# Kernel optimization log

Hardware: AMD Instinct MI355X
Metric: run time of the kernel (lower is better)

## Reference

```python
import jax, jax.numpy as jnp
import numpy as np

BETA = 0.95
THR = 1.0  # snntorch Leaky default threshold

# Heaviside spike with ATan surrogate gradient (snntorch default, alpha=2):
# d/dx = 1 / (1 + (pi*x)^2)
@jax.custom_vjp
def spike_fn(x):
    return (x > 0).astype(x.dtype)

def _spike_fwd(x):
    return spike_fn(x), x

def _spike_bwd(x, g):
    return (g / (1.0 + (jnp.pi * x) ** 2),)

spike_fn.defvjp(_spike_fwd, _spike_bwd)


def setup_inputs() -> dict:
    key = jax.random.key(0)
    ks = jax.random.split(key, 5)
    T, B, D_in, D_h, D_out = 25, 4096, 784, 1000, 10
    x = jax.random.normal(ks[0], (T, B, D_in), dtype=jnp.float32)
    # Kaiming-uniform-ish init like nn.Linear
    w1 = jax.random.uniform(ks[1], (D_h, D_in), jnp.float32, -1, 1) / np.sqrt(D_in)
    b1 = jax.random.uniform(ks[2], (D_h,), jnp.float32, -1, 1) / np.sqrt(D_in)
    w2 = jax.random.uniform(ks[3], (D_out, D_h), jnp.float32, -1, 1) / np.sqrt(D_h)
    b2 = jax.random.uniform(ks[4], (D_out,), jnp.float32, -1, 1) / np.sqrt(D_h)
    return {"x": x, "w1": w1, "b1": b1, "w2": w2, "b2": b2}


def reference(x, w1, b1, w2, b2):
    B = x.shape[1]
    mem1_0 = jnp.zeros((B, w1.shape[0]), x.dtype)
    mem2_0 = jnp.zeros((B, w2.shape[0]), x.dtype)

    def step(carry, xt):
        mem1, mem2 = carry
        # layer 1: Linear + Leaky (reset-by-subtraction, reset from prior mem)
        cur1 = xt @ w1.T + b1
        reset1 = spike_fn(mem1 - THR)
        mem1 = BETA * mem1 + cur1 - reset1 * THR
        spk1 = spike_fn(mem1 - THR)
        # layer 2
        cur2 = spk1 @ w2.T + b2
        reset2 = spike_fn(mem2 - THR)
        mem2 = BETA * mem2 + cur2 - reset2 * THR
        spk2 = spike_fn(mem2 - THR)
        return (mem1, mem2), spk2

    (mem1, mem2), spk_rec = jax.lax.scan(step, (mem1_0, mem2_0), x)
    return spk_rec, mem2
```

## Files before the change

### kernel.cpp

```cpp
#include <hip/hip_runtime.h>

typedef _Float16 f16;
typedef _Float16 f16x4 __attribute__((ext_vector_type(4)));
typedef _Float16 f16x8 __attribute__((ext_vector_type(8)));
typedef float f32x4 __attribute__((ext_vector_type(4)));

#define T_STEPS 25
#define BATCH   4096
#define DIN     784
#define DH      1000
#define HP      1024
#define DOUT    10
#define MROWS   (T_STEPS * BATCH)
#define KSEG    800
#define KA      (2 * KSEG)
#define KB      (3 * KSEG)
#define NTILES  (KB / 32)

__global__ void aconv_kernel(const float* __restrict__ x, f16* __restrict__ Ah)
{
    const int total = MROWS * 200;
    for (int idx = blockIdx.x * blockDim.x + threadIdx.x; idx < total;
         idx += gridDim.x * blockDim.x) {
        const int r  = idx / 200;
        const int c4 = (idx - r * 200) * 4;
        f16x4 hi, lo;
        if (c4 < DIN) {
            const float4 v = *(const float4*)(x + (size_t)r * DIN + c4);
            const float vv[4] = {v.x, v.y, v.z, v.w};
            #pragma unroll
            for (int j = 0; j < 4; ++j) {
                f16 h = (f16)vv[j];
                hi[j] = h;
                lo[j] = (f16)(vv[j] - (float)h);
            }
        } else {
            #pragma unroll
            for (int j = 0; j < 4; ++j) { hi[j] = (f16)0.f; lo[j] = (f16)0.f; }
        }
        *(f16x4*)(Ah + (size_t)r * KA + c4)        = hi;
        *(f16x4*)(Ah + (size_t)r * KA + KSEG + c4) = lo;
    }
}

__global__ void wconv_kernel(const float* __restrict__ w1, const float* __restrict__ b1,
                             const float* __restrict__ w2,
                             f16* __restrict__ Wh, float* __restrict__ b1p,
                             float* __restrict__ w2t)
{
    const int stride = gridDim.x * blockDim.x;
    const int tid0 = blockIdx.x * blockDim.x + threadIdx.x;
    for (int idx = tid0; idx < HP * KB; idx += stride) {
        const int n  = idx / KB;
        const int k  = idx - n * KB;
        const int seg = k / KSEG;
        const int kc  = k - seg * KSEG;
        float w = (n < DH && kc < DIN) ? w1[n * DIN + kc] : 0.f;
        f16 h = (f16)w;
        Wh[idx] = (seg < 2) ? h : (f16)(w - (float)h);
    }
    for (int idx = tid0; idx < HP; idx += stride)
        b1p[idx] = (idx < DH) ? b1[idx] : 0.f;
    for (int idx = tid0; idx < HP * DOUT; idx += stride) {
        const int h = idx / DOUT;
        const int o = idx - h * DOUT;
        w2t[idx] = (h < DH) ? w2[o * DH + h] : 0.f;
    }
}

#define GL(gp, ldsoff) __builtin_amdgcn_global_load_lds( \
    (const __attribute__((address_space(1))) void*)(gp), \
    (__attribute__((address_space(3))) void*)(lds + (ldsoff)), 16, 0, 0)

#define STAGE_A(tt) do { \
    const int ak_ = (((tt) < 50) ? (tt) : ((tt) - 50)) * 32; \
    GL(Ag + ak_,            ((tt) & 3) * 8192 + widoff); \
    GL(Ag + ak_ + 128 * KA, ((tt) & 3) * 8192 + 4096 + widoff); } while (0)
#define STAGE_B(tt) do { \
    const int bk_ = (tt) * 32; \
    GL(Bg + bk_,                     32768 + ((tt) & 3) * 8192 + widoff); \
    GL(Bg + bk_ + (size_t)128 * KB,  32768 + ((tt) & 3) * 8192 + 4096 + widoff); } while (0)

#define MFMA16(A0, A1, A2, A3, M0) \
    acc[M0+0][0] = __builtin_amdgcn_mfma_f32_16x16x32_f16(A0, bf0, acc[M0+0][0], 0, 0, 0); \
    acc[M0+0][1] = __builtin_amdgcn_mfma_f32_16x16x32_f16(A0, bf1, acc[M0+0][1], 0, 0, 0); \
    acc[M0+0][2] = __builtin_amdgcn_mfma_f32_16x16x32_f16(A0, bf2, acc[M0+0][2], 0, 0, 0); \
    acc[M0+0][3] = __builtin_amdgcn_mfma_f32_16x16x32_f16(A0, bf3, acc[M0+0][3], 0, 0, 0); \
    acc[M0+1][0] = __builtin_amdgcn_mfma_f32_16x16x32_f16(A1, bf0, acc[M0+1][0], 0, 0, 0); \
    acc[M0+1][1] = __builtin_amdgcn_mfma_f32_16x16x32_f16(A1, bf1, acc[M0+1][1], 0, 0, 0); \
    acc[M0+1][2] = __builtin_amdgcn_mfma_f32_16x16x32_f16(A1, bf2, acc[M0+1][2], 0, 0, 0); \
    acc[M0+1][3] = __builtin_amdgcn_mfma_f32_16x16x32_f16(A1, bf3, acc[M0+1][3], 0, 0, 0); \
    acc[M0+2][0] = __builtin_amdgcn_mfma_f32_16x16x32_f16(A2, bf0, acc[M0+2][0], 0, 0, 0); \
    acc[M0+2][1] = __builtin_amdgcn_mfma_f32_16x16x32_f16(A2, bf1, acc[M0+2][1], 0, 0, 0); \
    acc[M0+2][2] = __builtin_amdgcn_mfma_f32_16x16x32_f16(A2, bf2, acc[M0+2][2], 0, 0, 0); \
    acc[M0+2][3] = __builtin_amdgcn_mfma_f32_16x16x32_f16(A2, bf3, acc[M0+2][3], 0, 0, 0); \
    acc[M0+3][0] = __builtin_amdgcn_mfma_f32_16x16x32_f16(A3, bf0, acc[M0+3][0], 0, 0, 0); \
    acc[M0+3][1] = __builtin_amdgcn_mfma_f32_16x16x32_f16(A3, bf1, acc[M0+3][1], 0, 0, 0); \
    acc[M0+3][2] = __builtin_amdgcn_mfma_f32_16x16x32_f16(A3, bf2, acc[M0+3][2], 0, 0, 0); \
    acc[M0+3][3] = __builtin_amdgcn_mfma_f32_16x16x32_f16(A3, bf3, acc[M0+3][3], 0, 0, 0);

#define BODY(tt, STG, WAITSTR) do { \
    const int bA = ((tt) & 3) * 8192; \
    const int bB = 32768 + ((tt) & 3) * 8192; \
    f16x8 af0, af1, af2, af3, af4, af5, af6, af7, bf0, bf1, bf2, bf3; \
    af0 = *(const f16x8*)(lds + bA + aoffb + 0 * 512); \
    af1 = *(const f16x8*)(lds + bA + aoffb + 1 * 512); \
    af2 = *(const f16x8*)(lds + bA + aoffb + 2 * 512); \
    af3 = *(const f16x8*)(lds + bA + aoffb + 3 * 512); \
    bf0 = *(const f16x8*)(lds + bB + boffb + 0 * 512); \
    bf1 = *(const f16x8*)(lds + bB + boffb + 1 * 512); \
    bf2 = *(const f16x8*)(lds + bB + boffb + 2 * 512); \
    bf3 = *(const f16x8*)(lds + bB + boffb + 3 * 512); \
    __builtin_amdgcn_sched_barrier(0); \
    af4 = *(const f16x8*)(lds + bA + aoffb + 4 * 512); \
    af5 = *(const f16x8*)(lds + bA + aoffb + 5 * 512); \
    af6 = *(const f16x8*)(lds + bA + aoffb + 6 * 512); \
    af7 = *(const f16x8*)(lds + bA + aoffb + 7 * 512); \
    __builtin_amdgcn_sched_barrier(0); \
    if (STG) { STAGE_A((tt) + 3); STAGE_B((tt) + 3); } \
    asm volatile("s_waitcnt lgkmcnt(4)" ::: "memory"); \
    __builtin_amdgcn_sched_barrier(0); \
    __builtin_amdgcn_s_setprio(1); \
    MFMA16(af0, af1, af2, af3, 0) \
    __builtin_amdgcn_s_setprio(0); \
    asm volatile("s_waitcnt lgkmcnt(0)" ::: "memory"); \
    __builtin_amdgcn_sched_barrier(0); \
    __builtin_amdgcn_s_setprio(1); \
    MFMA16(af4, af5, af6, af7, 4) \
    __builtin_amdgcn_s_setprio(0); \
    asm volatile(WAITSTR ::: "memory"); \
    __builtin_amdgcn_s_barrier(); \
} while (0)

__global__ __launch_bounds__(512, 2)
void gemm_kernel(const f16* __restrict__ A, const f16* __restrict__ B,
                 const float* __restrict__ bias, float* __restrict__ C)
{
    __shared__ f16 lds[65536];

    const int bid = blockIdx.x;
    const int swz = (bid & 7) * 200 + (bid >> 3);
    const int mt = swz >> 2;
    const int nt = swz & 3;
    const size_t rowBase = (size_t)mt * 256;
    const int colBase = nt * 256;

    const int tid  = threadIdx.x;
    const int wid  = tid >> 6;
    const int lane = tid & 63;
    const int wm = wid >> 2;
    const int wn = wid & 3;

    const int srow = tid >> 2;
    const int g = (tid & 3) ^ ((tid >> 3) & 3);
    const f16* Ag = A + (rowBase + srow) * KA + g * 8;
    const f16* Bg = B + (size_t)(colBase + srow) * KB + g * 8;
    const int widoff = wid * 512;

    const int cq = (lane >> 4) ^ (((lane & 15) >> 1) & 3);
    const int aoffb = (wm * 128 + (lane & 15)) * 32 + cq * 8;
    const int boffb = (wn * 64  + (lane & 15)) * 32 + cq * 8;

    f32x4 acc[8][4];
    #pragma unroll
    for (int m = 0; m < 8; ++m)
        #pragma unroll
        for (int n = 0; n < 4; ++n)
            acc[m][n] = (f32x4){0.f, 0.f, 0.f, 0.f};

    STAGE_A(0); STAGE_B(0);
    STAGE_A(1); STAGE_B(1);
    STAGE_A(2); STAGE_B(2);
    asm volatile("s_waitcnt vmcnt(8)" ::: "memory");
    __builtin_amdgcn_s_barrier();

    #pragma unroll 2
    for (int t = 0; t < NTILES - 3; ++t)
        BODY(t, 1, "s_waitcnt vmcnt(8)");
    BODY(NTILES - 3, 0, "s_waitcnt vmcnt(4)");
    BODY(NTILES - 2, 0, "s_waitcnt vmcnt(0)");
    BODY(NTILES - 1, 0, "");

    const int c_col0 = colBase + wn * 64 + (lane & 15);
    const size_t c_row0 = rowBase + wm * 128 + (lane >> 4) * 4;
    #pragma unroll
    for (int n = 0; n < 4; ++n) {
        const int gcol = c_col0 + n * 16;
        const float bv = bias[gcol];
        #pragma unroll
        for (int m = 0; m < 8; ++m) {
            const size_t grow = c_row0 + m * 16;
            #pragma unroll
            for (int r = 0; r < 4; ++r)
                C[(grow + r) * HP + gcol] = acc[m][n][r] + bv;
        }
    }
}

__global__ __launch_bounds__(256)
void phase2_kernel(const float* __restrict__ cur1, const float* __restrict__ w2t,
                   const float* __restrict__ b2, float* __restrict__ out)
{
    __shared__ float w2s[HP * DOUT];
    const int tid = threadIdx.x;
    for (int i = tid; i < HP * DOUT; i += 256) w2s[i] = w2t[i];

    const int lane = tid & 63;
    const int wave = tid >> 6;
    const int b = blockIdx.x * 4 + wave;

    float m1[16];
    #pragma unroll
    for (int i = 0; i < 16; ++i) m1[i] = 0.f;
    float m2[DOUT], b2r[DOUT];
    #pragma unroll
    for (int o = 0; o < DOUT; ++o) { m2[o] = 0.f; b2r[o] = b2[o]; }
    __syncthreads();

    for (int t = 0; t < T_STEPS; ++t) {
        const float* cr = cur1 + ((size_t)t * BATCH + b) * HP;
        float p[DOUT];
        #pragma unroll
        for (int o = 0; o < DOUT; ++o) p[o] = 0.f;

        #pragma unroll
        for (int c = 0; c < 4; ++c) {
            const float4 cu = *(const float4*)(cr + c * 256 + lane * 4);
            const float cv[4] = {cu.x, cu.y, cu.z, cu.w};
            #pragma unroll
            for (int j = 0; j < 4; ++j) {
                const float mo = m1[c * 4 + j];
                const float rs = (mo > 1.0f) ? 1.0f : 0.0f;
                const float mn = 0.95f * mo + cv[j] - rs;
                m1[c * 4 + j] = mn;
                if (mn > 1.0f) {
                    const float* wr = w2s + (c * 256 + lane * 4 + j) * DOUT;
                    #pragma unroll
                    for (int o = 0; o < DOUT; ++o) p[o] += wr[o];
                }
            }
        }
        #pragma unroll
        for (int o = 0; o < DOUT; ++o) {
            float v = p[o];
            #pragma unroll
            for (int msk = 32; msk > 0; msk >>= 1) v += __shfl_xor(v, msk, 64);
            p[o] = v;
        }
        #pragma unroll
        for (int o = 0; o < DOUT; ++o) {
            const float cur2 = p[o] + b2r[o];
            const float mo = m2[o];
            const float rs = (mo > 1.0f) ? 1.0f : 0.0f;
            m2[o] = 0.95f * mo + cur2 - rs;
        }
        if (lane < DOUT)
            out[(size_t)t * (BATCH * DOUT) + (size_t)b * DOUT + lane] =
                (m2[lane] > 1.0f) ? 1.0f : 0.0f;
    }
    if (lane < DOUT)
        out[(size_t)T_STEPS * BATCH * DOUT + (size_t)b * DOUT + lane] = m2[lane];
}

extern "C" void kernel_launch(void* const* d_in, const int* in_sizes, int n_in,
                              void* d_out, int out_size, void* d_ws, size_t ws_size,
                              hipStream_t stream)
{
    const float* x  = (const float*)d_in[0];
    const float* w1 = (const float*)d_in[1];
    const float* b1 = (const float*)d_in[2];
    const float* w2 = (const float*)d_in[3];
    const float* b2 = (const float*)d_in[4];
    float* out = (float*)d_out;

    char* wsb = (char*)d_ws;
    f16*   Ah   = (f16*)(wsb);
    f16*   Wh   = (f16*)(wsb + 327680000);
    float* cur1 = (float*)(wsb + 327680000 + 4915200);
    float* b1p  = (float*)(wsb + 327680000 + 4915200 + 419430400);
    float* w2t  = (float*)(wsb + 327680000 + 4915200 + 419430400 + 4096);

    aconv_kernel<<<4096, 256, 0, stream>>>(x, Ah);
    wconv_kernel<<<1024, 256, 0, stream>>>(w1, b1, w2, Wh, b1p, w2t);
    gemm_kernel<<<1600, 512, 0, stream>>>(Ah, Wh, b1p, cur1);
    phase2_kernel<<<1024, 256, 0, stream>>>(cur1, w2t, b2, out);
}
```

Before: 778.2 us.

## Prefetch next tile's LDS fragments into double-buffered registers during MFMAs

Restructures the GEMM main loop so each iteration issues the first half of the next K-tile's A and B fragment loads from LDS right after the barrier, overlapping them with the second MFMA batch of the current tile. Two register sets alternate through a loop unrolled by two, and a peeled epilogue handles the last tile. The aim is to hide LDS read latency behind MFMA work. It costs 16 extra f16x8 registers per thread, which adds register pressure under the 512-thread, 2-blocks launch bound.

Result: no change. 772.0 us (-0.8%).

```diff
diff --git a/kernel.cpp b/kernel.cpp
--- a/kernel.cpp
+++ b/kernel.cpp
@@ -81,56 +81,60 @@
     GL(Bg + bk_,                     32768 + ((tt) & 3) * 8192 + widoff); \
     GL(Bg + bk_ + (size_t)128 * KB,  32768 + ((tt) & 3) * 8192 + 4096 + widoff); } while (0)
 
-#define MFMA16(A0, A1, A2, A3, M0) \
-    acc[M0+0][0] = __builtin_amdgcn_mfma_f32_16x16x32_f16(A0, bf0, acc[M0+0][0], 0, 0, 0); \
-    acc[M0+0][1] = __builtin_amdgcn_mfma_f32_16x16x32_f16(A0, bf1, acc[M0+0][1], 0, 0, 0); \
-    acc[M0+0][2] = __builtin_amdgcn_mfma_f32_16x16x32_f16(A0, bf2, acc[M0+0][2], 0, 0, 0); \
-    acc[M0+0][3] = __builtin_amdgcn_mfma_f32_16x16x32_f16(A0, bf3, acc[M0+0][3], 0, 0, 0); \
-    acc[M0+1][0] = __builtin_amdgcn_mfma_f32_16x16x32_f16(A1, bf0, acc[M0+1][0], 0, 0, 0); \
-    acc[M0+1][1] = __builtin_amdgcn_mfma_f32_16x16x32_f16(A1, bf1, acc[M0+1][1], 0, 0, 0); \
-    acc[M0+1][2] = __builtin_amdgcn_mfma_f32_16x16x32_f16(A1, bf2, acc[M0+1][2], 0, 0, 0); \
-    acc[M0+1][3] = __builtin_amdgcn_mfma_f32_16x16x32_f16(A1, bf3, acc[M0+1][3], 0, 0, 0); \
-    acc[M0+2][0] = __builtin_amdgcn_mfma_f32_16x16x32_f16(A2, bf0, acc[M0+2][0], 0, 0, 0); \
-    acc[M0+2][1] = __builtin_amdgcn_mfma_f32_16x16x32_f16(A2, bf1, acc[M0+2][1], 0, 0, 0); \
-    acc[M0+2][2] = __builtin_amdgcn_mfma_f32_16x16x32_f16(A2, bf2, acc[M0+2][2], 0, 0, 0); \
-    acc[M0+2][3] = __builtin_amdgcn_mfma_f32_16x16x32_f16(A2, bf3, acc[M0+2][3], 0, 0, 0); \
-    acc[M0+3][0] = __builtin_amdgcn_mfma_f32_16x16x32_f16(A3, bf0, acc[M0+3][0], 0, 0, 0); \
-    acc[M0+3][1] = __builtin_amdgcn_mfma_f32_16x16x32_f16(A3, bf1, acc[M0+3][1], 0, 0, 0); \
-    acc[M0+3][2] = __builtin_amdgcn_mfma_f32_16x16x32_f16(A3, bf2, acc[M0+3][2], 0, 0, 0); \
-    acc[M0+3][3] = __builtin_amdgcn_mfma_f32_16x16x32_f16(A3, bf3, acc[M0+3][3], 0, 0, 0);
-
-#define BODY(tt, STG, WAITSTR) do { \
-    const int bA = ((tt) & 3) * 8192; \
-    const int bB = 32768 + ((tt) & 3) * 8192; \
-    f16x8 af0, af1, af2, af3, af4, af5, af6, af7, bf0, bf1, bf2, bf3; \
-    af0 = *(const f16x8*)(lds + bA + aoffb + 0 * 512); \
-    af1 = *(const f16x8*)(lds + bA + aoffb + 1 * 512); \
-    af2 = *(const f16x8*)(lds + bA + aoffb + 2 * 512); \
-    af3 = *(const f16x8*)(lds + bA + aoffb + 3 * 512); \
-    bf0 = *(const f16x8*)(lds + bB + boffb + 0 * 512); \
-    bf1 = *(const f16x8*)(lds + bB + boffb + 1 * 512); \
-    bf2 = *(const f16x8*)(lds + bB + boffb + 2 * 512); \
-    bf3 = *(const f16x8*)(lds + bB + boffb + 3 * 512); \
+#define MFMA16(A0, A1, A2, A3, B0, B1, B2, B3, M0) \
+    acc[M0+0][0] = __builtin_amdgcn_mfma_f32_16x16x32_f16(A0, B0, acc[M0+0][0], 0, 0, 0); \
+    acc[M0+0][1] = __builtin_amdgcn_mfma_f32_16x16x32_f16(A0, B1, acc[M0+0][1], 0, 0, 0); \
+    acc[M0+0][2] = __builtin_amdgcn_mfma_f32_16x16x32_f16(A0, B2, acc[M0+0][2], 0, 0, 0); \
+    acc[M0+0][3] = __builtin_amdgcn_mfma_f32_16x16x32_f16(A0, B3, acc[M0+0][3], 0, 0, 0); \
+    acc[M0+1][0] = __builtin_amdgcn_mfma_f32_16x16x32_f16(A1, B0, acc[M0+1][0], 0, 0, 0); \
+    acc[M0+1][1] = __builtin_amdgcn_mfma_f32_16x16x32_f16(A1, B1, acc[M0+1][1], 0, 0, 0); \
+    acc[M0+1][2] = __builtin_amdgcn_mfma_f32_16x16x32_f16(A1, B2, acc[M0+1][2], 0, 0, 0); \
+    acc[M0+1][3] = __builtin_amdgcn_mfma_f32_16x16x32_f16(A1, B3, acc[M0+1][3], 0, 0, 0); \
+    acc[M0+2][0] = __builtin_amdgcn_mfma_f32_16x16x32_f16(A2, B0, acc[M0+2][0], 0, 0, 0); \
+    acc[M0+2][1] = __builtin_amdgcn_mfma_f32_16x16x32_f16(A2, B1, acc[M0+2][1], 0, 0, 0); \
+    acc[M0+2][2] = __builtin_amdgcn_mfma_f32_16x16x32_f16(A2, B2, acc[M0+2][2], 0, 0, 0); \
+    acc[M0+2][3] = __builtin_amdgcn_mfma_f32_16x16x32_f16(A2, B3, acc[M0+2][3], 0, 0, 0); \
+    acc[M0+3][0] = __builtin_amdgcn_mfma_f32_16x16x32_f16(A3, B0, acc[M0+3][0], 0, 0, 0); \
+    acc[M0+3][1] = __builtin_amdgcn_mfma_f32_16x16x32_f16(A3, B1, acc[M0+3][1], 0, 0, 0); \
+    acc[M0+3][2] = __builtin_amdgcn_mfma_f32_16x16x32_f16(A3, B2, acc[M0+3][2], 0, 0, 0); \
+    acc[M0+3][3] = __builtin_amdgcn_mfma_f32_16x16x32_f16(A3, B3, acc[M0+3][3], 0, 0, 0);
+
+#define BODY(tt, aI0,aI1,aI2,aI3, bI0,bI1,bI2,bI3, aO0,aO1,aO2,aO3, bO0,bO1,bO2,bO3, STG, VMWSTR) do { \
+    const int bcur = ((tt) & 3) * 8192; \
+    const int bnxt = (((tt) + 1) & 3) * 8192; \
+    if (STG) { STAGE_A((tt) + 3); STAGE_B((tt) + 3); } \
+    asm volatile("s_waitcnt lgkmcnt(0)" ::: "memory");    \
     __builtin_amdgcn_sched_barrier(0); \
-    af4 = *(const f16x8*)(lds + bA + aoffb + 4 * 512); \
-    af5 = *(const f16x8*)(lds + bA + aoffb + 5 * 512); \
-    af6 = *(const f16x8*)(lds + bA + aoffb + 6 * 512); \
-    af7 = *(const f16x8*)(lds + bA + aoffb + 7 * 512); \
-    __builtin_amdgcn_sched_barrier(0); \
-    if (STG) { STAGE_A((tt) + 3); STAGE_B((tt) + 3); } \
-    asm volatile("s_waitcnt lgkmcnt(4)" ::: "memory"); \
+    ah0 = *(const f16x8*)(lds + bcur + aoffb + 4 * 512); \
+    ah1 = *(const f16x8*)(lds + bcur + aoffb + 5 * 512); \
+    ah2 = *(const f16x8*)(lds + bcur + aoffb + 6 * 512); \
+    ah3 = *(const f16x8*)(lds + bcur + aoffb + 7 * 512); \
     __builtin_amdgcn_sched_barrier(0); \
     __builtin_amdgcn_s_setprio(1); \
-    MFMA16(af0, af1, af2, af3, 0) \
+    MFMA16(aI0, aI1, aI2, aI3, bI0, bI1, bI2, bI3, 0)     \
     __builtin_amdgcn_s_setprio(0); \
-    asm volatile("s_waitcnt lgkmcnt(0)" ::: "memory"); \
+    asm volatile("s_waitcnt lgkmcnt(0)" ::: "memory");    \
+    __builtin_amdgcn_sched_barrier(0); \
+    asm volatile(VMWSTR ::: "memory"); \
+    __builtin_amdgcn_s_barrier();                         \
+    aO0 = *(const f16x8*)(lds + bnxt + aoffb + 0 * 512); \
+    aO1 = *(const f16x8*)(lds + bnxt + aoffb + 1 * 512); \
+    aO2 = *(const f16x8*)(lds + bnxt + aoffb + 2 * 512); \
+    aO3 = *(const f16x8*)(lds + bnxt + aoffb + 3 * 512); \
+    bO0 = *(const f16x8*)(lds + 32768 + bnxt + boffb + 0 * 512); \
+    bO1 = *(const f16x8*)(lds + 32768 + bnxt + boffb + 1 * 512); \
+    bO2 = *(const f16x8*)(lds + 32768 + bnxt + boffb + 2 * 512); \
+    bO3 = *(const f16x8*)(lds + 32768 + bnxt + boffb + 3 * 512); \
     __builtin_amdgcn_sched_barrier(0); \
     __builtin_amdgcn_s_setprio(1); \
-    MFMA16(af4, af5, af6, af7, 4) \
+    MFMA16(ah0, ah1, ah2, ah3, bI0, bI1, bI2, bI3, 4)     \
     __builtin_amdgcn_s_setprio(0); \
-    asm volatile(WAITSTR ::: "memory"); \
-    __builtin_amdgcn_s_barrier(); \
 } while (0)
+
+#define BODY_(...) BODY(__VA_ARGS__)
+
+#define SET_A aA0,aA1,aA2,aA3, bA0,bA1,bA2,bA3
+#define SET_B aB0,aB1,aB2,aB3, bB0,bB1,bB2,bB3
 
 __global__ __launch_bounds__(512, 2)
 void gemm_kernel(const f16* __restrict__ A, const f16* __restrict__ B,
@@ -168,18 +172,44 @@
         for (int n = 0; n < 4; ++n)
             acc[m][n] = (f32x4){0.f, 0.f, 0.f, 0.f};
 
+    f16x8 aA0, aA1, aA2, aA3, bA0, bA1, bA2, bA3;
+    f16x8 aB0, aB1, aB2, aB3, bB0, bB1, bB2, bB3;
+    f16x8 ah0, ah1, ah2, ah3;
+
     STAGE_A(0); STAGE_B(0);
     STAGE_A(1); STAGE_B(1);
     STAGE_A(2); STAGE_B(2);
     asm volatile("s_waitcnt vmcnt(8)" ::: "memory");
     __builtin_amdgcn_s_barrier();
-
-    #pragma unroll 2
-    for (int t = 0; t < NTILES - 3; ++t)
-        BODY(t, 1, "s_waitcnt vmcnt(8)");
-    BODY(NTILES - 3, 0, "s_waitcnt vmcnt(4)");
-    BODY(NTILES - 2, 0, "s_waitcnt vmcnt(0)");
-    BODY(NTILES - 1, 0, "");
+    aA0 = *(const f16x8*)(lds + aoffb + 0 * 512);
+    aA1 = *(const f16x8*)(lds + aoffb + 1 * 512);
+    aA2 = *(const f16x8*)(lds + aoffb + 2 * 512);
+    aA3 = *(const f16x8*)(lds + aoffb + 3 * 512);
+    bA0 = *(const f16x8*)(lds + 32768 + boffb + 0 * 512);
+    bA1 = *(const f16x8*)(lds + 32768 + boffb + 1 * 512);
+    bA2 = *(const f16x8*)(lds + 32768 + boffb + 2 * 512);
+    bA3 = *(const f16x8*)(lds + 32768 + boffb + 3 * 512);
+
+    for (int t = 0; t < NTILES - 3; t += 2) {
+        BODY_(t,     SET_A, SET_B, 1, "s_waitcnt vmcnt(8)");
+        BODY_(t + 1, SET_B, SET_A, 1, "s_waitcnt vmcnt(8)");
+    }
+    BODY_(NTILES - 3, SET_A, SET_B, 0, "s_waitcnt vmcnt(4)");
+    BODY_(NTILES - 2, SET_B, SET_A, 0, "s_waitcnt vmcnt(0)");
+    {
+        const int bcur = ((NTILES - 1) & 3) * 8192;
+        asm volatile("s_waitcnt lgkmcnt(0)" ::: "memory");
+        __builtin_amdgcn_sched_barrier(0);
+        ah0 = *(const f16x8*)(lds + bcur + aoffb + 4 * 512);
+        ah1 = *(const f16x8*)(lds + bcur + aoffb + 5 * 512);
+        ah2 = *(const f16x8*)(lds + bcur + aoffb + 6 * 512);
+        ah3 = *(const f16x8*)(lds + bcur + aoffb + 7 * 512);
+        __builtin_amdgcn_sched_barrier(0);
+        MFMA16(aA0, aA1, aA2, aA3, bA0, bA1, bA2, bA3, 0)
+        asm volatile("s_waitcnt lgkmcnt(0)" ::: "memory");
+        __builtin_amdgcn_sched_barrier(0);
+        MFMA16(ah0, ah1, ah2, ah3, bA0, bA1, bA2, bA3, 4)
+    }
 
     const int c_col0 = colBase + wn * 64 + (lane & 15);
     const size_t c_row0 = rowBase + wm * 128 + (lane >> 4) * 4;
```
